# Optimization experiments

Measured on AMD Instinct MI355X. Metric: run time of the kernel, lower is better.

## Reference

```python
import jax, jax.numpy as jnp
import numpy as np

B, S, D, E, K = 4, 2048, 1024, 8, 2
LN_EPS = 1e-5


def setup_inputs() -> dict:
    key = jax.random.key(0)
    ks = jax.random.split(key, 8)
    s = 1.0 / np.sqrt(D)
    return {
        "x": jax.random.normal(ks[0], (B, S, D), dtype=jnp.float32),
        "noise": jax.random.normal(ks[1], (B, S, E), dtype=jnp.float32) * (1.0 / E),
        "W_route": jax.random.uniform(ks[2], (D, E), minval=-s, maxval=s, dtype=jnp.float32),
        "b_route": jax.random.uniform(ks[3], (E,), minval=-s, maxval=s, dtype=jnp.float32),
        "ln_gamma": jnp.ones((E,), dtype=jnp.float32),
        "ln_beta": jnp.zeros((E,), dtype=jnp.float32),
        "W_exp": jax.random.uniform(ks[4], (E, D, D), minval=-s, maxval=s, dtype=jnp.float32),
        "b_exp": jax.random.uniform(ks[5], (E, D), minval=-s, maxval=s, dtype=jnp.float32),
    }


def reference(x, noise, W_route, b_route, ln_gamma, ln_beta, W_exp, b_exp):
    # Routing: Linear(dim, E) -> LayerNorm(E) -> softmax, plus noise
    logits = jnp.einsum("bsd,de->bse", x, W_route) + b_route
    mu = logits.mean(axis=-1, keepdims=True)
    var = logits.var(axis=-1, keepdims=True)
    ln = (logits - mu) / jnp.sqrt(var + LN_EPS) * ln_gamma + ln_beta
    routing = jax.nn.softmax(ln, axis=-1) + noise

    topk_w, topk_i = jax.lax.top_k(routing, K)          # [B,S,K]
    topk_w = jax.nn.softmax(topk_w, axis=-1)

    # Dense all-expert compute (faithful to the naive original)
    expert_out = jnp.einsum("bsd,edf->bsef", x, W_exp) + b_exp  # [B,S,E,D]

    # Gather top-k experts per token and combine
    sel = jnp.take_along_axis(expert_out, topk_i[..., None], axis=2)  # [B,S,K,D]
    return (sel * topk_w[..., None]).sum(axis=2)
```

## Files before the change

kernel.cpp:

```cpp
#include <hip/hip_runtime.h>
#include <hip/hip_bf16.h>


typedef unsigned short u16;
typedef __bf16 bf16x8 __attribute__((ext_vector_type(8)));
typedef float floatx4 __attribute__((ext_vector_type(4)));
typedef unsigned short u16x8 __attribute__((ext_vector_type(8)));
typedef unsigned short u16x4 __attribute__((ext_vector_type(4)));

#define NTOK 8192
#define DDIM 1024
#define NEXP 8

__device__ __forceinline__ u16 f2bf(float f) {
    union { float f; unsigned int i; } c; c.f = f;
    unsigned int i = c.i;
    return (u16)((i + 0x7fffu + ((i >> 16) & 1u)) >> 16);
}

__device__ __forceinline__ void gl2l16(const u16* g, u16* l) {
    __builtin_amdgcn_global_load_lds(
        (const __attribute__((address_space(1))) unsigned int*)g,
        (__attribute__((address_space(3))) unsigned int*)l, 16, 0, 0);
}

__global__ __launch_bounds__(256) void transpose_w(const float* __restrict__ W,
                                                   u16* __restrict__ WT) {
    __shared__ float tileT[64 * 65];
    const int e = blockIdx.z, d0 = blockIdx.y * 64, f0 = blockIdx.x * 64;
    const int t = threadIdx.x;
    const float* src = W + (size_t)e * DDIM * DDIM;
    u16* dst = WT + (size_t)e * DDIM * DDIM;
    const int r = t >> 2, q = t & 3;
    const float* sp = src + (size_t)(d0 + r) * DDIM + f0 + q * 16;
#pragma unroll
    for (int j = 0; j < 4; ++j) {
        float4 v = *(const float4*)(sp + j * 4);
        int c = q * 16 + j * 4;
        tileT[(c + 0) * 65 + r] = v.x;
        tileT[(c + 1) * 65 + r] = v.y;
        tileT[(c + 2) * 65 + r] = v.z;
        tileT[(c + 3) * 65 + r] = v.w;
    }
    __syncthreads();
    const int c2 = t >> 2, dq = (t & 3) * 16;
    u16x8 o0, o1;
#pragma unroll
    for (int i = 0; i < 8; ++i) o0[i] = f2bf(tileT[c2 * 65 + dq + i]);
#pragma unroll
    for (int i = 0; i < 8; ++i) o1[i] = f2bf(tileT[c2 * 65 + dq + 8 + i]);
    u16* dp = dst + (size_t)(f0 + c2) * DDIM + d0 + dq;
    *(u16x8*)dp = o0;
    *(u16x8*)(dp + 8) = o1;
}

__global__ __launch_bounds__(256) void routing_compute(
    const float* __restrict__ x, const float* __restrict__ noise,
    const float* __restrict__ Wr, const float* __restrict__ br,
    const float* __restrict__ gamma, const float* __restrict__ beta,
    int* __restrict__ e01, float2* __restrict__ w01,
    u16* __restrict__ xb, int wxb) {
    __shared__ __align__(16) float wrT[NEXP][DDIM];
    const int t = threadIdx.x;
#pragma unroll
    for (int i = 0; i < 8; ++i) {
        int f4 = i * 256 + t;
        int d = f4 >> 1, half = (f4 & 1) * 4;
        float4 v = *(const float4*)&Wr[d * 8 + half];
        wrT[half + 0][d] = v.x; wrT[half + 1][d] = v.y;
        wrT[half + 2][d] = v.z; wrT[half + 3][d] = v.w;
    }
    __syncthreads();

    const int wave = t >> 6, lane = t & 63;
    const int tok = blockIdx.x * 4 + wave;
    const float4* xrow = (const float4*)(x + (size_t)tok * DDIM);
    u16* xbrow = xb + (size_t)tok * DDIM;
    float acc[8];
#pragma unroll
    for (int e = 0; e < 8; ++e) acc[e] = 0.f;
#pragma unroll
    for (int i = 0; i < 4; ++i) {
        int d4 = i * 64 + lane;
        float4 xv = xrow[d4];
        if (wxb) {
            u16x4 b;
            b[0] = f2bf(xv.x); b[1] = f2bf(xv.y);
            b[2] = f2bf(xv.z); b[3] = f2bf(xv.w);
            *(u16x4*)(xbrow + d4 * 4) = b;
        }
#pragma unroll
        for (int e = 0; e < 8; ++e) {
            float4 wv = *(const float4*)&wrT[e][d4 * 4];
            acc[e] += xv.x * wv.x + xv.y * wv.y + xv.z * wv.z + xv.w * wv.w;
        }
    }
#pragma unroll
    for (int off = 32; off >= 1; off >>= 1) {
#pragma unroll
        for (int e = 0; e < 8; ++e) acc[e] += __shfl_xor(acc[e], off, 64);
    }
    if (lane == 0) {
        float lg[8], mu = 0.f;
#pragma unroll
        for (int e = 0; e < 8; ++e) { lg[e] = acc[e] + br[e]; mu += lg[e]; }
        mu *= 0.125f;
        float var = 0.f;
#pragma unroll
        for (int e = 0; e < 8; ++e) { float d = lg[e] - mu; var += d * d; }
        var *= 0.125f;
        float rstd = rsqrtf(var + 1e-5f);
        float ln[8], mx = -1e30f;
#pragma unroll
        for (int e = 0; e < 8; ++e) {
            ln[e] = (lg[e] - mu) * rstd * gamma[e] + beta[e];
            mx = fmaxf(mx, ln[e]);
        }
        float s = 0.f, p[8];
#pragma unroll
        for (int e = 0; e < 8; ++e) { p[e] = expf(ln[e] - mx); s += p[e]; }
        float inv = 1.f / s, r[8];
#pragma unroll
        for (int e = 0; e < 8; ++e) r[e] = p[e] * inv + noise[(size_t)tok * 8 + e];
        int i0 = 0; float v0 = r[0];
#pragma unroll
        for (int e = 1; e < 8; ++e) if (r[e] > v0) { v0 = r[e]; i0 = e; }
        int i1 = -1; float v1 = -1e30f;
#pragma unroll
        for (int e = 0; e < 8; ++e) if (e != i0 && r[e] > v1) { v1 = r[e]; i1 = e; }
        float w0 = 1.f / (1.f + expf(v1 - v0));
        e01[tok] = i0 | (i1 << 8);
        w01[tok] = make_float2(w0, 1.f - w0);
    }
}

__global__ __launch_bounds__(256) void build_lists(
    const int* __restrict__ e01, const float2* __restrict__ w01,
    int* __restrict__ counts, int* __restrict__ list_tok, float* __restrict__ list_w) {
    const int g = blockIdx.x;
    const int slot = g >> 3, ex = g & 7;
    const int t = threadIdx.x, wave = t >> 6, lane = t & 63;
    __shared__ int wtot[4];
    int base = 0;
    for (int start = 0; start < NTOK; start += 256) {
        int tok = start + t;
        int packed = e01[tok];
        int e = slot ? ((packed >> 8) & 0xff) : (packed & 0xff);
        bool sel = (e == ex);
        unsigned long long m = __ballot(sel);
        int prefix = __popcll(m & ((1ULL << lane) - 1ULL));
        if (lane == 0) wtot[wave] = __popcll(m);
        __syncthreads();
        int wbase = 0;
#pragma unroll
        for (int wv = 0; wv < 4; ++wv) if (wv < wave) wbase += wtot[wv];
        int total = wtot[0] + wtot[1] + wtot[2] + wtot[3];
        if (sel) {
            float2 w2 = w01[tok];
            int pos = base + wbase + prefix;
            list_tok[g * NTOK + pos] = tok;
            list_w[g * NTOK + pos] = slot ? w2.y : w2.x;
        }
        base += total;
        __syncthreads();
    }
    if (t == 0) counts[g] = base;
}

__global__ __launch_bounds__(256, 3) void moe_gemm_bf16(
    const u16* __restrict__ xb, const u16* __restrict__ WT,
    const float* __restrict__ bexp, const int* __restrict__ counts,
    const int* __restrict__ list_tok, const float* __restrict__ list_w,
    float* __restrict__ out0, float* __restrict__ out1,
    int merged, int grp_base, int accum) {
    const int id = blockIdx.x;
    int e, slot, n, m;
    if (merged) {
        e = id & 7; slot = (id >> 3) & 1; n = (id >> 4) & 7; m = id >> 7;
    } else {
        e = id & 7; slot = 0; n = (id >> 3) & 7; m = id >> 6;
    }
    const int grp = merged ? ((slot << 3) | e) : (grp_base + e);
    float* const out = (merged && slot) ? out1 : out0;
    int cnt = counts[grp];
    cnt = cnt < 0 ? 0 : (cnt > NTOK ? NTOK : cnt);
    const int m0 = m * 128;
    if (m0 >= cnt) return;
    const int n0 = n * 128;

    __shared__ __align__(16) u16 A_s[128 * 64];
    __shared__ __align__(16) u16 B_s[128 * 64];
    __shared__ int tok_s[128];
    __shared__ float w_s[128];
    __shared__ float bias_s[128];

    const int t = threadIdx.x;
    if (t < 128) {
        int r = m0 + t;
        int rr = r < cnt ? r : cnt - 1;
        tok_s[t] = list_tok[grp * NTOK + rr] & (NTOK - 1);
        w_s[t] = (r < cnt) ? list_w[grp * NTOK + rr] : 0.f;
        bias_s[t] = bexp[e * DDIM + n0 + t];
    }
    __syncthreads();

    const int wave = t >> 6, lane = t & 63;
    const int sr = t >> 3, ch = t & 7;
    const u16* ag[4];
    const u16* bg[4];
#pragma unroll
    for (int s = 0; s < 4; ++s) {
        int row = s * 32 + sr;
        int cs = ((ch ^ (row & 7)) << 3);
        ag[s] = xb + (size_t)tok_s[row] * DDIM + cs;
        bg[s] = WT + ((size_t)e * DDIM + n0 + row) * DDIM + cs;
    }
    u16* const al = A_s + wave * 512;
    u16* const bl = B_s + wave * 512;

    const int wm = wave >> 1, wn = wave & 1;
    const int lm = lane & 15, kc = lane >> 4;

    floatx4 acc[4][4];
#pragma unroll
    for (int mi = 0; mi < 4; ++mi)
#pragma unroll
        for (int ni = 0; ni < 4; ++ni) acc[mi][ni] = (floatx4){0.f, 0.f, 0.f, 0.f};

    for (int kk = 0; kk < DDIM; kk += 64) {
        if (kk) __syncthreads();
#pragma unroll
        for (int s = 0; s < 4; ++s) {
            gl2l16(ag[s] + kk, al + s * 2048);
            gl2l16(bg[s] + kk, bl + s * 2048);
        }
        __syncthreads();
#pragma unroll
        for (int ks = 0; ks < 2; ++ks) {
            const int c = (((ks * 4 + kc) ^ (lm & 7)) << 3);
            bf16x8 af[4], bfr[4];
#pragma unroll
            for (int mi = 0; mi < 4; ++mi)
                af[mi] = *(const bf16x8*)&A_s[(wm * 64 + mi * 16 + lm) * 64 + c];
#pragma unroll
            for (int ni = 0; ni < 4; ++ni)
                bfr[ni] = *(const bf16x8*)&B_s[(wn * 64 + ni * 16 + lm) * 64 + c];
#pragma unroll
            for (int mi = 0; mi < 4; ++mi)
#pragma unroll
                for (int ni = 0; ni < 4; ++ni)
                    acc[mi][ni] = __builtin_amdgcn_mfma_f32_16x16x32_bf16(
                        af[mi], bfr[ni], acc[mi][ni], 0, 0, 0);
        }
    }

#pragma unroll
    for (int mi = 0; mi < 4; ++mi) {
        int rb = wm * 64 + mi * 16 + (lane >> 4) * 4;
#pragma unroll
        for (int reg = 0; reg < 4; ++reg) {
            int r = rb + reg;
            if (m0 + r < cnt) {
                size_t tok = (size_t)tok_s[r];
                float w = w_s[r];
                float* yrow = out + tok * DDIM + n0;
#pragma unroll
                for (int ni = 0; ni < 4; ++ni) {
                    int col = wn * 64 + ni * 16 + lm;
                    float v = w * (acc[mi][ni][reg] + bias_s[col]);
                    if (accum) v += yrow[col];
                    yrow[col] = v;
                }
            }
        }
    }
}

__global__ __launch_bounds__(256) void combine_add(const float* __restrict__ a,
                                                   float* __restrict__ o, int n4) {
    int stride = gridDim.x * 256;
    for (int i = blockIdx.x * 256 + threadIdx.x; i < n4; i += stride) {
        float4 va = ((const float4*)a)[i];
        float4 vo = ((float4*)o)[i];
        vo.x += va.x; vo.y += va.y; vo.z += va.z; vo.w += va.w;
        ((float4*)o)[i] = vo;
    }
}

__global__ __launch_bounds__(256) void moe_gemm_f32(
    const float* __restrict__ xf, const u16* __restrict__ WT,
    const float* __restrict__ bexp, const int* __restrict__ counts,
    const int* __restrict__ list_tok, const float* __restrict__ list_w,
    float* __restrict__ out, int grp_base, int accum) {
    const int id = blockIdx.x;
    const int e = id & 7;
    const int n = (id >> 3) & 7;
    const int m = id >> 6;
    const int grp = grp_base + e;
    int cnt = counts[grp];
    cnt = cnt < 0 ? 0 : (cnt > NTOK ? NTOK : cnt);
    const int m0 = m * 128;
    if (m0 >= cnt) return;
    const int n0 = n * 128;

    __shared__ __align__(16) u16 A_s[128 * 64];
    __shared__ __align__(16) u16 B_s[128 * 64];
    __shared__ int tok_s[128];
    __shared__ float w_s[128];
    __shared__ float bias_s[128];

    const int t = threadIdx.x;
    if (t < 128) {
        int r = m0 + t;
        int rr = r < cnt ? r : cnt - 1;
        tok_s[t] = list_tok[grp * NTOK + rr] & (NTOK - 1);
        w_s[t] = (r < cnt) ? list_w[grp * NTOK + rr] : 0.f;
        bias_s[t] = bexp[e * DDIM + n0 + t];
    }
    __syncthreads();

    const int sr = t >> 3;
    const int ch = t & 7;
    const int co = ch * 8;

    size_t arow[4];
    u16 *adst[4], *bdst[4];
#pragma unroll
    for (int s = 0; s < 4; ++s) {
        int row = s * 32 + sr;
        arow[s] = (size_t)tok_s[row] * DDIM + co;
        int cs = ((ch ^ (row & 7)) << 3);
        adst[s] = A_s + row * 64 + cs;
        bdst[s] = B_s + row * 64 + cs;
    }
    const u16* bsrc = WT + ((size_t)e * DDIM + n0 + sr) * DDIM + co;

    const int lane = t & 63, wave = t >> 6;
    const int wm = wave >> 1, wn = wave & 1;
    const int lm = lane & 15, kc = lane >> 4;

    floatx4 acc[4][4];
#pragma unroll
    for (int mi = 0; mi < 4; ++mi)
#pragma unroll
        for (int ni = 0; ni < 4; ++ni) acc[mi][ni] = (floatx4){0.f, 0.f, 0.f, 0.f};

    u16x8 pb[4];
    float4 pfa[4][2];
#pragma unroll
    for (int s = 0; s < 4; ++s) {
        pfa[s][0] = *(const float4*)(xf + arow[s]);
        pfa[s][1] = *(const float4*)(xf + arow[s] + 4);
        pb[s] = *(const u16x8*)(bsrc + (size_t)s * 32 * DDIM);
    }

    for (int kk = 0; kk < DDIM; kk += 64) {
        u16x8 wa[4];
#pragma unroll
        for (int s = 0; s < 4; ++s) {
            wa[s][0] = f2bf(pfa[s][0].x); wa[s][1] = f2bf(pfa[s][0].y);
            wa[s][2] = f2bf(pfa[s][0].z); wa[s][3] = f2bf(pfa[s][0].w);
            wa[s][4] = f2bf(pfa[s][1].x); wa[s][5] = f2bf(pfa[s][1].y);
            wa[s][6] = f2bf(pfa[s][1].z); wa[s][7] = f2bf(pfa[s][1].w);
        }
        __syncthreads();
#pragma unroll
        for (int s = 0; s < 4; ++s) {
            *(u16x8*)adst[s] = wa[s];
            *(u16x8*)bdst[s] = pb[s];
        }
        __syncthreads();
        const int nk = kk + 64;
        if (nk < DDIM) {
#pragma unroll
            for (int s = 0; s < 4; ++s) {
                pfa[s][0] = *(const float4*)(xf + arow[s] + nk);
                pfa[s][1] = *(const float4*)(xf + arow[s] + nk + 4);
                pb[s] = *(const u16x8*)(bsrc + (size_t)s * 32 * DDIM + nk);
            }
        }
#pragma unroll
        for (int ks = 0; ks < 2; ++ks) {
            bf16x8 af[4], bfr[4];
#pragma unroll
            for (int mi = 0; mi < 4; ++mi) {
                int row = wm * 64 + mi * 16 + lm;
                int c = (((ks * 4 + kc) ^ (row & 7)) << 3);
                af[mi] = *(const bf16x8*)&A_s[row * 64 + c];
            }
#pragma unroll
            for (int ni = 0; ni < 4; ++ni) {
                int row = wn * 64 + ni * 16 + lm;
                int c = (((ks * 4 + kc) ^ (row & 7)) << 3);
                bfr[ni] = *(const bf16x8*)&B_s[row * 64 + c];
            }
#pragma unroll
            for (int mi = 0; mi < 4; ++mi)
#pragma unroll
                for (int ni = 0; ni < 4; ++ni)
                    acc[mi][ni] = __builtin_amdgcn_mfma_f32_16x16x32_bf16(
                        af[mi], bfr[ni], acc[mi][ni], 0, 0, 0);
        }
    }

#pragma unroll
    for (int mi = 0; mi < 4; ++mi) {
        int rb = wm * 64 + mi * 16 + (lane >> 4) * 4;
#pragma unroll
        for (int reg = 0; reg < 4; ++reg) {
            int r = rb + reg;
            if (m0 + r < cnt) {
                size_t tok = (size_t)tok_s[r];
                float w = w_s[r];
                float* yrow = out + tok * DDIM + n0;
#pragma unroll
                for (int ni = 0; ni < 4; ++ni) {
                    int col = wn * 64 + ni * 16 + lm;
                    float v = w * (acc[mi][ni][reg] + bias_s[col]);
                    if (accum) v += yrow[col];
                    yrow[col] = v;
                }
            }
        }
    }
}

extern "C" void kernel_launch(void* const* d_in, const int* in_sizes, int n_in,
                              void* d_out, int out_size, void* d_ws, size_t ws_size,
                              hipStream_t stream) {
    const float* x     = (const float*)d_in[0];
    const float* noise = (const float*)d_in[1];
    const float* Wr    = (const float*)d_in[2];
    const float* br    = (const float*)d_in[3];
    const float* gamma = (const float*)d_in[4];
    const float* beta  = (const float*)d_in[5];
    const float* Wexp  = (const float*)d_in[6];
    const float* bexp  = (const float*)d_in[7];
    float* out = (float*)d_out;

    unsigned char* ws = (unsigned char*)d_ws;
    u16* WT       = (u16*)ws;
    int* counts   = (int*)(ws + 16777216);
    int* list_tok = (int*)(ws + 16777472);
    float* list_w = (float*)(ws + 17301760);
    int* e01      = (int*)(ws + 17826048);
    float2* w01   = (float2*)(ws + 17858816);
    u16* xb       = (u16*)(ws + 17924352);
    float* out1   = (float*)(ws + 34701568);
    const size_t need_bf16   = 34701568;
    const size_t need_merged = 34701568 + 33554432;

    const int have_bf16 = ws_size >= need_bf16;

    routing_compute<<<NTOK / 4, 256, 0, stream>>>(x, noise, Wr, br, gamma, beta,
                                                  e01, w01, xb, have_bf16);
    build_lists<<<16, 256, 0, stream>>>(e01, w01, counts, list_tok, list_w);
    transpose_w<<<dim3(16, 16, 8), 256, 0, stream>>>(Wexp, WT);

    if (ws_size >= need_merged) {
        moe_gemm_bf16<<<dim3(8192), 256, 0, stream>>>(
            xb, WT, bexp, counts, list_tok, list_w, out, out1, 1, 0, 0);
        combine_add<<<2048, 256, 0, stream>>>(out1, out, NTOK * DDIM / 4);
    } else if (have_bf16) {
        moe_gemm_bf16<<<dim3(4096), 256, 0, stream>>>(
            xb, WT, bexp, counts, list_tok, list_w, out, out, 0, 0, 0);
        moe_gemm_bf16<<<dim3(4096), 256, 0, stream>>>(
            xb, WT, bexp, counts, list_tok, list_w, out, out, 0, 8, 1);
    } else {
        moe_gemm_f32<<<dim3(4096), 256, 0, stream>>>(
            x, WT, bexp, counts, list_tok, list_w, out, 0, 0);
        moe_gemm_f32<<<dim3(4096), 256, 0, stream>>>(
            x, WT, bexp, counts, list_tok, list_w, out, 8, 1);
    }
}
```

Baseline: 213.2 us.

## Fuse routing and weight transpose into one launch, prefetch in list build

Merges the routing kernel and the expert weight transpose/bf16 conversion into a single launch, with blocks split by index, so both memory-bound phases run concurrently and one launch is removed. build_lists now prefetches the next chunk of packed expert ids to hide load latency. The GEMM launch bounds go from 3 to 4 waves per SIMD minimum, which caps register use and may cause spills. The transpose blocks now reserve the larger shared-memory footprint of the routing blocks, which lowers their occupancy.

```diff
diff --git a/kernel.cpp b/kernel.cpp
--- a/kernel.cpp
+++ b/kernel.cpp
@@ -24,113 +24,117 @@
         (__attribute__((address_space(3))) unsigned int*)l, 16, 0, 0);
 }
 
-__global__ __launch_bounds__(256) void transpose_w(const float* __restrict__ W,
-                                                   u16* __restrict__ WT) {
-    __shared__ float tileT[64 * 65];
-    const int e = blockIdx.z, d0 = blockIdx.y * 64, f0 = blockIdx.x * 64;
-    const int t = threadIdx.x;
-    const float* src = W + (size_t)e * DDIM * DDIM;
-    u16* dst = WT + (size_t)e * DDIM * DDIM;
-    const int r = t >> 2, q = t & 3;
-    const float* sp = src + (size_t)(d0 + r) * DDIM + f0 + q * 16;
-#pragma unroll
-    for (int j = 0; j < 4; ++j) {
-        float4 v = *(const float4*)(sp + j * 4);
-        int c = q * 16 + j * 4;
-        tileT[(c + 0) * 65 + r] = v.x;
-        tileT[(c + 1) * 65 + r] = v.y;
-        tileT[(c + 2) * 65 + r] = v.z;
-        tileT[(c + 3) * 65 + r] = v.w;
-    }
-    __syncthreads();
-    const int c2 = t >> 2, dq = (t & 3) * 16;
-    u16x8 o0, o1;
-#pragma unroll
-    for (int i = 0; i < 8; ++i) o0[i] = f2bf(tileT[c2 * 65 + dq + i]);
-#pragma unroll
-    for (int i = 0; i < 8; ++i) o1[i] = f2bf(tileT[c2 * 65 + dq + 8 + i]);
-    u16* dp = dst + (size_t)(f0 + c2) * DDIM + d0 + dq;
-    *(u16x8*)dp = o0;
-    *(u16x8*)(dp + 8) = o1;
-}
-
-__global__ __launch_bounds__(256) void routing_compute(
+__global__ __launch_bounds__(256) void routing_and_transpose(
     const float* __restrict__ x, const float* __restrict__ noise,
     const float* __restrict__ Wr, const float* __restrict__ br,
     const float* __restrict__ gamma, const float* __restrict__ beta,
+    const float* __restrict__ W,
     int* __restrict__ e01, float2* __restrict__ w01,
-    u16* __restrict__ xb, int wxb) {
-    __shared__ __align__(16) float wrT[NEXP][DDIM];
+    u16* __restrict__ xb, u16* __restrict__ WT, int wxb) {
+    __shared__ __align__(16) float smem[NEXP * DDIM];
     const int t = threadIdx.x;
-#pragma unroll
-    for (int i = 0; i < 8; ++i) {
-        int f4 = i * 256 + t;
-        int d = f4 >> 1, half = (f4 & 1) * 4;
-        float4 v = *(const float4*)&Wr[d * 8 + half];
-        wrT[half + 0][d] = v.x; wrT[half + 1][d] = v.y;
-        wrT[half + 2][d] = v.z; wrT[half + 3][d] = v.w;
-    }
-    __syncthreads();
-
-    const int wave = t >> 6, lane = t & 63;
-    const int tok = blockIdx.x * 4 + wave;
-    const float4* xrow = (const float4*)(x + (size_t)tok * DDIM);
-    u16* xbrow = xb + (size_t)tok * DDIM;
-    float acc[8];
-#pragma unroll
-    for (int e = 0; e < 8; ++e) acc[e] = 0.f;
-#pragma unroll
-    for (int i = 0; i < 4; ++i) {
-        int d4 = i * 64 + lane;
-        float4 xv = xrow[d4];
-        if (wxb) {
-            u16x4 b;
-            b[0] = f2bf(xv.x); b[1] = f2bf(xv.y);
-            b[2] = f2bf(xv.z); b[3] = f2bf(xv.w);
-            *(u16x4*)(xbrow + d4 * 4) = b;
-        }
-#pragma unroll
-        for (int e = 0; e < 8; ++e) {
-            float4 wv = *(const float4*)&wrT[e][d4 * 4];
-            acc[e] += xv.x * wv.x + xv.y * wv.y + xv.z * wv.z + xv.w * wv.w;
-        }
-    }
-#pragma unroll
-    for (int off = 32; off >= 1; off >>= 1) {
-#pragma unroll
-        for (int e = 0; e < 8; ++e) acc[e] += __shfl_xor(acc[e], off, 64);
-    }
-    if (lane == 0) {
-        float lg[8], mu = 0.f;
-#pragma unroll
-        for (int e = 0; e < 8; ++e) { lg[e] = acc[e] + br[e]; mu += lg[e]; }
-        mu *= 0.125f;
-        float var = 0.f;
-#pragma unroll
-        for (int e = 0; e < 8; ++e) { float d = lg[e] - mu; var += d * d; }
-        var *= 0.125f;
-        float rstd = rsqrtf(var + 1e-5f);
-        float ln[8], mx = -1e30f;
-#pragma unroll
-        for (int e = 0; e < 8; ++e) {
-            ln[e] = (lg[e] - mu) * rstd * gamma[e] + beta[e];
-            mx = fmaxf(mx, ln[e]);
-        }
-        float s = 0.f, p[8];
-#pragma unroll
-        for (int e = 0; e < 8; ++e) { p[e] = expf(ln[e] - mx); s += p[e]; }
-        float inv = 1.f / s, r[8];
-#pragma unroll
-        for (int e = 0; e < 8; ++e) r[e] = p[e] * inv + noise[(size_t)tok * 8 + e];
-        int i0 = 0; float v0 = r[0];
-#pragma unroll
-        for (int e = 1; e < 8; ++e) if (r[e] > v0) { v0 = r[e]; i0 = e; }
-        int i1 = -1; float v1 = -1e30f;
-#pragma unroll
-        for (int e = 0; e < 8; ++e) if (e != i0 && r[e] > v1) { v1 = r[e]; i1 = e; }
-        float w0 = 1.f / (1.f + expf(v1 - v0));
-        e01[tok] = i0 | (i1 << 8);
-        w01[tok] = make_float2(w0, 1.f - w0);
+
+    if (blockIdx.x < 2048) {
+        float (*wrT)[DDIM] = (float(*)[DDIM])smem;
+#pragma unroll
+        for (int i = 0; i < 8; ++i) {
+            int f4 = i * 256 + t;
+            int d = f4 >> 1, half = (f4 & 1) * 4;
+            float4 v = *(const float4*)&Wr[d * 8 + half];
+            wrT[half + 0][d] = v.x; wrT[half + 1][d] = v.y;
+            wrT[half + 2][d] = v.z; wrT[half + 3][d] = v.w;
+        }
+        __syncthreads();
+
+        const int wave = t >> 6, lane = t & 63;
+        const int tok = blockIdx.x * 4 + wave;
+        const float4* xrow = (const float4*)(x + (size_t)tok * DDIM);
+        u16* xbrow = xb + (size_t)tok * DDIM;
+        float acc[8];
+#pragma unroll
+        for (int e = 0; e < 8; ++e) acc[e] = 0.f;
+#pragma unroll
+        for (int i = 0; i < 4; ++i) {
+            int d4 = i * 64 + lane;
+            float4 xv = xrow[d4];
+            if (wxb) {
+                u16x4 b;
+                b[0] = f2bf(xv.x); b[1] = f2bf(xv.y);
+                b[2] = f2bf(xv.z); b[3] = f2bf(xv.w);
+                *(u16x4*)(xbrow + d4 * 4) = b;
+            }
+#pragma unroll
+            for (int e = 0; e < 8; ++e) {
+                float4 wv = *(const float4*)&wrT[e][d4 * 4];
+                acc[e] += xv.x * wv.x + xv.y * wv.y + xv.z * wv.z + xv.w * wv.w;
+            }
+        }
+#pragma unroll
+        for (int off = 32; off >= 1; off >>= 1) {
+#pragma unroll
+            for (int e = 0; e < 8; ++e) acc[e] += __shfl_xor(acc[e], off, 64);
+        }
+        if (lane == 0) {
+            float lg[8], mu = 0.f;
+#pragma unroll
+            for (int e = 0; e < 8; ++e) { lg[e] = acc[e] + br[e]; mu += lg[e]; }
+            mu *= 0.125f;
+            float var = 0.f;
+#pragma unroll
+            for (int e = 0; e < 8; ++e) { float d = lg[e] - mu; var += d * d; }
+            var *= 0.125f;
+            float rstd = rsqrtf(var + 1e-5f);
+            float ln[8], mx = -1e30f;
+#pragma unroll
+            for (int e = 0; e < 8; ++e) {
+                ln[e] = (lg[e] - mu) * rstd * gamma[e] + beta[e];
+                mx = fmaxf(mx, ln[e]);
+            }
+            float s = 0.f, p[8];
+#pragma unroll
+            for (int e = 0; e < 8; ++e) { p[e] = expf(ln[e] - mx); s += p[e]; }
+            float inv = 1.f / s, r[8];
+#pragma unroll
+            for (int e = 0; e < 8; ++e)
+                r[e] = p[e] * inv + noise[(size_t)tok * 8 + e];
+            int i0 = 0; float v0 = r[0];
+#pragma unroll
+            for (int e = 1; e < 8; ++e) if (r[e] > v0) { v0 = r[e]; i0 = e; }
+            int i1 = -1; float v1 = -1e30f;
+#pragma unroll
+            for (int e = 0; e < 8; ++e)
+                if (e != i0 && r[e] > v1) { v1 = r[e]; i1 = e; }
+            float w0 = 1.f / (1.f + expf(v1 - v0));
+            e01[tok] = i0 | (i1 << 8);
+            w01[tok] = make_float2(w0, 1.f - w0);
+        }
+    } else {
+        float* tileT = smem;
+        const int id2 = blockIdx.x - 2048;
+        const int e = id2 >> 8, d0 = ((id2 >> 4) & 15) * 64, f0 = (id2 & 15) * 64;
+        const float* src = W + (size_t)e * DDIM * DDIM;
+        u16* dst = WT + (size_t)e * DDIM * DDIM;
+        const int r = t >> 2, q = t & 3;
+        const float* sp = src + (size_t)(d0 + r) * DDIM + f0 + q * 16;
+#pragma unroll
+        for (int j = 0; j < 4; ++j) {
+            float4 v = *(const float4*)(sp + j * 4);
+            int c = q * 16 + j * 4;
+            tileT[(c + 0) * 65 + r] = v.x;
+            tileT[(c + 1) * 65 + r] = v.y;
+            tileT[(c + 2) * 65 + r] = v.z;
+            tileT[(c + 3) * 65 + r] = v.w;
+        }
+        __syncthreads();
+        const int c2 = t >> 2, dq = (t & 3) * 16;
+        u16x8 o0, o1;
+#pragma unroll
+        for (int i = 0; i < 8; ++i) o0[i] = f2bf(tileT[c2 * 65 + dq + i]);
+#pragma unroll
+        for (int i = 0; i < 8; ++i) o1[i] = f2bf(tileT[c2 * 65 + dq + 8 + i]);
+        u16* dp = dst + (size_t)(f0 + c2) * DDIM + d0 + dq;
+        *(u16x8*)dp = o0;
+        *(u16x8*)(dp + 8) = o1;
     }
 }
 
@@ -142,9 +146,10 @@
     const int t = threadIdx.x, wave = t >> 6, lane = t & 63;
     __shared__ int wtot[4];
     int base = 0;
+    int packed = e01[t];
     for (int start = 0; start < NTOK; start += 256) {
+        int nxt = (start + 256 < NTOK) ? e01[start + 256 + t] : 0;
         int tok = start + t;
-        int packed = e01[tok];
         int e = slot ? ((packed >> 8) & 0xff) : (packed & 0xff);
         bool sel = (e == ex);
         unsigned long long m = __ballot(sel);
@@ -163,11 +168,12 @@
         }
         base += total;
         __syncthreads();
+        packed = nxt;
     }
     if (t == 0) counts[g] = base;
 }
 
-__global__ __launch_bounds__(256, 3) void moe_gemm_bf16(
+__global__ __launch_bounds__(256, 4) void moe_gemm_bf16(
     const u16* __restrict__ xb, const u16* __restrict__ WT,
     const float* __restrict__ bexp, const int* __restrict__ counts,
     const int* __restrict__ list_tok, const float* __restrict__ list_w,
@@ -452,10 +458,9 @@
 
     const int have_bf16 = ws_size >= need_bf16;
 
-    routing_compute<<<NTOK / 4, 256, 0, stream>>>(x, noise, Wr, br, gamma, beta,
-                                                  e01, w01, xb, have_bf16);
+    routing_and_transpose<<<4096, 256, 0, stream>>>(
+        x, noise, Wr, br, gamma, beta, Wexp, e01, w01, xb, WT, have_bf16);
     build_lists<<<16, 256, 0, stream>>>(e01, w01, counts, list_tok, list_w);
-    transpose_w<<<dim3(16, 16, 8), 256, 0, stream>>>(Wexp, WT);
 
     if (ws_size >= need_merged) {
         moe_gemm_bf16<<<dim3(8192), 256, 0, stream>>>(
```

After: 210.2 us (median of 2 runs). No clear change (-1.4%).
